# Kernel tuning notes

Measured on AMD Instinct MI355X. Metric: run time of the kernel, lower is better.

## Reference

```python
import jax, jax.numpy as jnp
import numpy as np

N_E = 8192
E_DIM = 64
BETA = 0.25
DIVERSITY_GAMMA = 1.0
INV_TEMP = 100.0
EPS = 1e-05


def _entropy(p):
    # matches torch: (-p * log(clamp(p, min=eps))).sum(-1)
    return (-p * jnp.log(jnp.clip(p, EPS))).sum(axis=-1)


def setup_inputs() -> dict:
    key = jax.random.key(0)
    k1, k2 = jax.random.split(key)
    z = jax.random.normal(k1, (16, E_DIM, 32, 32), dtype=jnp.float32)
    # codebook, init like nn.Embedding then uniform_(-1/n_e, 1/n_e) scale doesn't matter for math;
    # use a small uniform init faithful to the module
    emb = jax.random.uniform(k2, (N_E, E_DIM), dtype=jnp.float32,
                             minval=-1.0 / N_E, maxval=1.0 / N_E)
    return {"z": z, "emb": emb}


def reference(z, emb):
    sg = jax.lax.stop_gradient
    # b c h w -> b h w c
    zp = jnp.transpose(z, (0, 2, 3, 1))            # [B,H,W,C]
    zf = zp.reshape(-1, E_DIM)                      # [N, C]
    # pairwise squared distances: ||z||^2 + ||e||^2 - 2 z e^T
    d = (jnp.sum(zf * zf, axis=1, keepdims=True)
         + jnp.sum(emb * emb, axis=1)
         - 2.0 * jnp.einsum('nd,kd->nk', zf, emb))  # [N, n_e]
    min_indices = jnp.argmin(d, axis=1)             # [N]
    z_q = emb[min_indices].reshape(zp.shape)        # gather, [B,H,W,C]
    # legacy commitment loss
    loss = (jnp.mean((sg(z_q) - zp) ** 2)
            + BETA * jnp.mean((z_q - sg(zp)) ** 2))
    # entropy aux loss (frac_per_sample_entropy == 1.0)
    prob = jax.nn.softmax(-d * INV_TEMP, axis=-1)   # [N, n_e]
    per_sample_entropy = _entropy(prob).mean()
    avg_prob = prob.mean(axis=0)                    # [n_e]
    codebook_entropy = _entropy(avg_prob)
    entropy_aux = per_sample_entropy - DIVERSITY_GAMMA * codebook_entropy
    # straight-through estimator
    z_q = zp + sg(z_q - zp)
    quantized = jnp.transpose(z_q, (0, 3, 1, 2))    # b h w c -> b c h w
    return quantized, loss, entropy_aux, min_indices
```

## Files before the change

### kernel.cpp

```cpp
#include <hip/hip_runtime.h>
#include <cfloat>


typedef __attribute__((ext_vector_type(8))) short short8v;
typedef __attribute__((ext_vector_type(4))) float f32x4;

#define C100L2E 144.26950408889634f
#define C200L2E 288.53900817779268f
#define LN2 0.6931471805599453

#define BLOB_TILE 33792
#define OFF_BLOB   0
#define OFF_INVZ   2162688
#define OFF_MINIDX 2228224
#define OFF_AVG    2293760
#define OFF_PSE    2326528
#define OFF_ZPART  2326544
#define OFF_S1PART (OFF_ZPART + 262144)
#define OFF_DMPART (OFF_S1PART + 262144)
#define OFF_IMPART (OFF_DMPART + 262144)
#define OFF_LOSSP  (OFF_IMPART + 262144)

__device__ __forceinline__ unsigned short f2bf_rne(float f) {
    unsigned u = __float_as_uint(f);
    u = (u + 0x7fffu + ((u >> 16) & 1u)) >> 16;
    return (unsigned short)u;
}

__device__ __forceinline__ void gload_lds16(const void* g, void* l) {
    __builtin_amdgcn_global_load_lds(
        (const __attribute__((address_space(1))) unsigned int*)g,
        (__attribute__((address_space(3))) unsigned int*)l, 16, 0, 0);
}

__global__ __launch_bounds__(256) void k_prep(const float* __restrict__ emb,
                                              char* __restrict__ blob) {
    const int k = blockIdx.x * 256 + threadIdx.x;
    const float* row = emb + k * 64;
    float fv[64];
#pragma unroll
    for (int i = 0; i < 16; ++i) {
        float4 v = ((const float4*)row)[i];
        fv[4 * i] = v.x; fv[4 * i + 1] = v.y; fv[4 * i + 2] = v.z; fv[4 * i + 3] = v.w;
    }
    float r8[8];
#pragma unroll
    for (int j = 0; j < 8; ++j) r8[j] = __fmul_rn(fv[j], fv[j]);
#pragma unroll
    for (int i = 8; i < 64; i += 8)
#pragma unroll
        for (int j = 0; j < 8; ++j)
            r8[j] = __fadd_rn(r8[j], __fmul_rn(fv[i + j], fv[i + j]));
    float s01 = __fadd_rn(r8[0], r8[1]), s23 = __fadd_rn(r8[2], r8[3]);
    float s45 = __fadd_rn(r8[4], r8[5]), s67 = __fadd_rn(r8[6], r8[7]);
    float e2 = __fadd_rn(__fadd_rn(s01, s23), __fadd_rn(s45, s67));

    char* tb = blob + (size_t)(k >> 7) * BLOB_TILE;
    const int r = k & 127;
    ((float*)(tb + 32768))[r] = e2;
    const int sw = (r & 7) << 4;
#pragma unroll
    for (int dh = 0; dh < 2; ++dh)
#pragma unroll
        for (int cg = 0; cg < 4; ++cg) {
            short8v hv, lv;
#pragma unroll
            for (int e = 0; e < 8; ++e) {
                float f = fv[dh * 32 + cg * 8 + e];
                unsigned short hb = f2bf_rne(f);
                float hf = __uint_as_float((unsigned)hb << 16);
                hv[e] = (short)hb;
                lv[e] = (short)f2bf_rne(f - hf);
            }
            const int byt = (r * 128 + dh * 64 + cg * 16) ^ sw;
            *(short8v*)(tb + byt) = hv;
            *(short8v*)(tb + 16384 + byt) = lv;
        }
}

#define STAGE_EMB(DSTBASE, TILE)                                                  \
    {                                                                             \
        const char* gsrc = blob + (size_t)(TILE) * BLOB_TILE;                     \
        char* ldst = (DSTBASE) + ((tid >> 6) << 10);                              \
        const char* g = gsrc + tid * 16;                                          \
        _Pragma("unroll")                                                         \
        for (int q = 0; q < 8; ++q)                                               \
            gload_lds16(g + q * 4096, ldst + q * 4096);                           \
        if (tid < 32) gload_lds16(gsrc + 32768 + tid * 16, (DSTBASE) + 32768);    \
    }

__global__ __launch_bounds__(256) void k_pass1(
    const float* __restrict__ z, const char* __restrict__ blob,
    char* __restrict__ zblob,
    float* __restrict__ Zpart, float* __restrict__ S1part,
    float* __restrict__ dmpart, int* __restrict__ impart)
{
    __shared__ __align__(16) char smem[BLOB_TILE];
    __shared__ float zzsh[64];
    float (*zt)[68] = (float (*)[68])smem;

    const int tid = threadIdx.x;
    const int panel = blockIdx.x >> 2;
    const int ks = blockIdx.x & 3;
    const int n0 = panel * 64;

    {
        const int c = tid & 63, rq = (tid >> 6) * 16;
        const float* src = z + ((n0 >> 10) * 64 + c) * 1024 + (n0 & 1023) + rq;
#pragma unroll
        for (int i = 0; i < 4; ++i) {
            float4 v = ((const float4*)src)[i];
            *(float4*)&zt[c][rq + 4 * i] = v;
        }
    }
    __syncthreads();
    if (tid < 64) {
        float r8[8];
#pragma unroll
        for (int j = 0; j < 8; ++j) { float v = zt[j][tid]; r8[j] = __fmul_rn(v, v); }
#pragma unroll
        for (int i = 8; i < 64; i += 8)
#pragma unroll
            for (int j = 0; j < 8; ++j) {
                float v = zt[i + j][tid];
                r8[j] = __fadd_rn(r8[j], __fmul_rn(v, v));
            }
        float s01 = __fadd_rn(r8[0], r8[1]), s23 = __fadd_rn(r8[2], r8[3]);
        float s45 = __fadd_rn(r8[4], r8[5]), s67 = __fadd_rn(r8[6], r8[7]);
        zzsh[tid] = __fadd_rn(__fadd_rn(s01, s23), __fadd_rn(s45, s67));
    }

    const int ln = tid & 63, wv = tid >> 6;
    const int lr = ln & 15, lg = ln >> 4;

    short8v Ah[2], Al[2];
#pragma unroll
    for (int s = 0; s < 2; ++s) {
        const int row = wv * 16 + lr;
        const int db = s * 32 + lg * 8;
#pragma unroll
        for (int j = 0; j < 8; ++j) {
            float f = zt[db + j][row];
            unsigned short hb = f2bf_rne(f);
            float hf = __uint_as_float((unsigned)hb << 16);
            Ah[s][j] = (short)hb;
            Al[s][j] = (short)f2bf_rne(f - hf);
        }
    }

    if (ks == 0) {
        char* tb = zblob + (size_t)panel * 16384;
        const int rowp = wv * 16 + lr;
#pragma unroll
        for (int s = 0; s < 2; ++s) {
            const int byt = rowp * 128 + s * 64 + lg * 16;
            *(short8v*)(tb + byt) = Ah[s];
            *(short8v*)(tb + 8192 + byt) = Al[s];
        }
    }
    __syncthreads();

    float zzr[4];
#pragma unroll
    for (int rg = 0; rg < 4; ++rg) zzr[rg] = zzsh[wv * 16 + lg * 4 + rg];

    STAGE_EMB(smem, ks * 16);

    float Zp[4] = {0.f, 0.f, 0.f, 0.f}, S1p[4] = {0.f, 0.f, 0.f, 0.f};
    float dmin[4] = {FLT_MAX, FLT_MAX, FLT_MAX, FLT_MAX};
    int imin[4] = {0, 0, 0, 0};

    for (int it = 0; it < 16; ++it) {
        const int kbase = ks * 2048 + it * 128;
        __syncthreads();

        f32x4 acc[8];
#pragma unroll
        for (int f = 0; f < 8; ++f) { f32x4 zv = {0.f, 0.f, 0.f, 0.f}; acc[f] = zv; }

#pragma unroll
        for (int f = 0; f < 8; ++f) {
            const int rr = f * 16 + lr;
            const int sw2 = (rr & 7) << 4;
            short8v Bh[2], Bl[2];
#pragma unroll
            for (int s = 0; s < 2; ++s) {
                const int byt = (rr * 128 + s * 64 + lg * 16) ^ sw2;
                Bh[s] = *(const short8v*)(smem + byt);
                Bl[s] = *(const short8v*)(smem + 16384 + byt);
            }
#pragma unroll
            for (int s = 0; s < 2; ++s) {
                acc[f] = __builtin_amdgcn_mfma_f32_16x16x32_bf16(Ah[s], Bh[s], acc[f], 0, 0, 0);
                acc[f] = __builtin_amdgcn_mfma_f32_16x16x32_bf16(Ah[s], Bl[s], acc[f], 0, 0, 0);
                acc[f] = __builtin_amdgcn_mfma_f32_16x16x32_bf16(Al[s], Bh[s], acc[f], 0, 0, 0);
                acc[f] = __builtin_amdgcn_mfma_f32_16x16x32_bf16(Al[s], Bl[s], acc[f], 0, 0, 0);
            }
        }

        float e2v[8];
#pragma unroll
        for (int f = 0; f < 8; ++f)
            e2v[f] = *(const float*)(smem + 32768 + (f * 16 + lr) * 4);

        __syncthreads();
        if (it < 15) STAGE_EMB(smem, ks * 16 + it + 1);

#pragma unroll
        for (int f = 0; f < 8; ++f) {
            const float c2 = e2v[f] * C100L2E;
            const int kk = kbase + f * 16 + lr;
#pragma unroll
            for (int rg = 0; rg < 4; ++rg) {
                const float sdot = acc[f][rg];
                const float t = fmaf(sdot, C200L2E, -c2);
                const float ex = __builtin_amdgcn_exp2f(t);
                Zp[rg] += ex;
                S1p[rg] = fmaf(t, ex, S1p[rg]);
                const float dnp = __fsub_rn(__fadd_rn(zzr[rg], e2v[f]),
                                            __fmul_rn(2.f, sdot));
                if (dnp < dmin[rg]) { dmin[rg] = dnp; imin[rg] = kk; }
            }
        }
    }

#pragma unroll
    for (int msk = 1; msk < 16; msk <<= 1) {
#pragma unroll
        for (int rg = 0; rg < 4; ++rg) {
            float d2 = __shfl_xor(dmin[rg], msk, 16);
            int i2 = __shfl_xor(imin[rg], msk, 16);
            float Z2 = __shfl_xor(Zp[rg], msk, 16);
            float s2 = __shfl_xor(S1p[rg], msk, 16);
            if (d2 < dmin[rg] || (d2 == dmin[rg] && i2 < imin[rg])) {
                dmin[rg] = d2; imin[rg] = i2;
            }
            Zp[rg] += Z2;
            S1p[rg] += s2;
        }
    }
    if (lr == 0) {
#pragma unroll
        for (int rg = 0; rg < 4; ++rg) {
            const int n = n0 + wv * 16 + lg * 4 + rg;
            Zpart[ks * 16384 + n] = Zp[rg];
            S1part[ks * 16384 + n] = S1p[rg];
            dmpart[ks * 16384 + n] = dmin[rg];
            impart[ks * 16384 + n] = imin[rg];
        }
    }
}

__global__ __launch_bounds__(256) void k_rowred(
    const float* __restrict__ Zpart, const float* __restrict__ S1part,
    const float* __restrict__ dmpart, const int* __restrict__ impart,
    float* __restrict__ invZ, int* __restrict__ minidx,
    float* __restrict__ out_idx, double* __restrict__ pse_sum)
{
    const int n = blockIdx.x * 256 + threadIdx.x;
    float Z = __fadd_rn(__fadd_rn(Zpart[n], Zpart[16384 + n]),
                        __fadd_rn(Zpart[32768 + n], Zpart[49152 + n]));
    float S1 = __fadd_rn(__fadd_rn(S1part[n], S1part[16384 + n]),
                         __fadd_rn(S1part[32768 + n], S1part[49152 + n]));
    float dm = dmpart[n];
    int im = impart[n];
#pragma unroll
    for (int ksp = 1; ksp < 4; ++ksp) {
        float d2 = dmpart[ksp * 16384 + n];
        int i2 = impart[ksp * 16384 + n];
        if (d2 < dm || (d2 == dm && i2 < im)) { dm = d2; im = i2; }
    }
    minidx[n] = im;
    out_idx[n] = (float)im;
    float iz = 1.0f / Z;
    invZ[n] = iz;
    double h = log((double)Z) - LN2 * (double)S1 * (double)iz;
#pragma unroll
    for (int m = 32; m > 0; m >>= 1) h += __shfl_xor(h, m, 64);
    if ((threadIdx.x & 63) == 0) atomicAdd(pse_sum, h);
}

__global__ __launch_bounds__(256) void k_pass2(
    const char* __restrict__ zblob, const char* __restrict__ blob,
    const float* __restrict__ invZ, float* __restrict__ avg_acc)
{
    __shared__ __align__(16) char smem[BLOB_TILE + 4096];
    float* izAll = (float*)(smem + BLOB_TILE);

    const int tid = threadIdx.x;
    const int kt = blockIdx.x & 63;
    const int ns = blockIdx.x >> 6;
    const int ln = tid & 63, wv = tid >> 6;
    const int lr = ln & 15, lg = ln >> 4;

    STAGE_EMB(smem, kt);
    gload_lds16((const char*)(invZ + ns * 1024) + tid * 16,
                (char*)izAll + (wv << 10));
    __syncthreads();

    float e2v[8];
#pragma unroll
    for (int f = 0; f < 8; ++f)
        e2v[f] = *(const float*)(smem + 32768 + (f * 16 + lr) * 4);

    float acck[8] = {0.f, 0.f, 0.f, 0.f, 0.f, 0.f, 0.f, 0.f};

    for (int it = 0; it < 8; ++it) {
        short8v Ah[2][2], Al[2][2];
        const int p64 = ns * 16 + it * 2 + (wv >> 1);
        const char* tb = zblob + (size_t)p64 * 16384;
#pragma unroll
        for (int m = 0; m < 2; ++m) {
            const int rowp = (wv & 1) * 32 + m * 16 + lr;
#pragma unroll
            for (int s = 0; s < 2; ++s) {
                const int byt = rowp * 128 + s * 64 + lg * 16;
                Ah[m][s] = *(const short8v*)(tb + byt);
                Al[m][s] = *(const short8v*)(tb + 8192 + byt);
            }
        }
        const int izb = it * 128 + wv * 32 + lg * 4;
        float4 iz0 = *(const float4*)&izAll[izb];
        float4 iz1 = *(const float4*)&izAll[izb + 16];
        float izr[2][4] = {{iz0.x, iz0.y, iz0.z, iz0.w},
                           {iz1.x, iz1.y, iz1.z, iz1.w}};

        f32x4 acc[2][8];
#pragma unroll
        for (int m = 0; m < 2; ++m)
#pragma unroll
            for (int f = 0; f < 8; ++f) {
                f32x4 zv = {0.f, 0.f, 0.f, 0.f};
                acc[m][f] = zv;
            }

#pragma unroll
        for (int f = 0; f < 8; ++f) {
            const int rr = f * 16 + lr;
            const int sw2 = (rr & 7) << 4;
            short8v Bh[2], Bl[2];
#pragma unroll
            for (int s = 0; s < 2; ++s) {
                const int byt = (rr * 128 + s * 64 + lg * 16) ^ sw2;
                Bh[s] = *(const short8v*)(smem + byt);
                Bl[s] = *(const short8v*)(smem + 16384 + byt);
            }
#pragma unroll
            for (int s = 0; s < 2; ++s)
#pragma unroll
                for (int m = 0; m < 2; ++m) {
                    acc[m][f] = __builtin_amdgcn_mfma_f32_16x16x32_bf16(Ah[m][s], Bh[s], acc[m][f], 0, 0, 0);
                    acc[m][f] = __builtin_amdgcn_mfma_f32_16x16x32_bf16(Ah[m][s], Bl[s], acc[m][f], 0, 0, 0);
                    acc[m][f] = __builtin_amdgcn_mfma_f32_16x16x32_bf16(Al[m][s], Bh[s], acc[m][f], 0, 0, 0);
                    acc[m][f] = __builtin_amdgcn_mfma_f32_16x16x32_bf16(Al[m][s], Bl[s], acc[m][f], 0, 0, 0);
                }
        }

#pragma unroll
        for (int f = 0; f < 8; ++f) {
            const float c2 = e2v[f] * C100L2E;
#pragma unroll
            for (int m = 0; m < 2; ++m)
#pragma unroll
                for (int rg = 0; rg < 4; ++rg) {
                    const float t = fmaf(acc[m][f][rg], C200L2E, -c2);
                    const float ex = __builtin_amdgcn_exp2f(t);
                    acck[f] = fmaf(ex, izr[m][rg], acck[f]);
                }
        }
    }

#pragma unroll
    for (int f = 0; f < 8; ++f) {
        float cs = acck[f];
        cs += __shfl_xor(cs, 16, 64);
        cs += __shfl_xor(cs, 32, 64);
        if (lg == 0) atomicAdd(&avg_acc[kt * 128 + f * 16 + lr], cs);
    }
}

__global__ __launch_bounds__(256) void k_quant(
    const float* __restrict__ z, const float* __restrict__ emb,
    const int* __restrict__ minidx, float* __restrict__ out,
    double* __restrict__ loss_part)
{
    __shared__ float lred[4];
    const int o = blockIdx.x * 256 + threadIdx.x;
    const int n = ((o >> 16) << 10) + (o & 1023);
    const int c = (o >> 10) & 63;
    const int idx = minidx[n];
    const float e = emb[idx * 64 + c];
    const float zv = z[o];
    out[o] = e;
    float d = e - zv;
    float sq = d * d;
#pragma unroll
    for (int m = 32; m > 0; m >>= 1) sq += __shfl_xor(sq, m, 64);
    if ((threadIdx.x & 63) == 0) lred[threadIdx.x >> 6] = sq;
    __syncthreads();
    if (threadIdx.x == 0)
        loss_part[blockIdx.x] = (double)lred[0] + (double)lred[1]
                              + (double)lred[2] + (double)lred[3];
}

__global__ __launch_bounds__(256) void k_final(
    const float* __restrict__ avg_acc, const double* __restrict__ pse_sum,
    const double* __restrict__ loss_part, float* __restrict__ out)
{
    __shared__ double red[256];
    const int tid = threadIdx.x;

    double lsum = 0.0;
    for (int k = tid; k < 4096; k += 256) lsum += loss_part[k];
    red[tid] = lsum;
    __syncthreads();
    for (int s = 128; s > 0; s >>= 1) {
        if (tid < s) red[tid] += red[tid + s];
        __syncthreads();
    }
    double ltot = red[0];
    __syncthreads();

    double local = 0.0;
    for (int k = tid; k < 8192; k += 256) {
        float p = avg_acc[k] * (1.0f / 16384.0f);
        float cl = fmaxf(p, 1e-5f);
        local += (double)(-p * logf(cl));
    }
    red[tid] = local;
    __syncthreads();
    for (int s = 128; s > 0; s >>= 1) {
        if (tid < s) red[tid] += red[tid + s];
        __syncthreads();
    }
    if (tid == 0) {
        double ce = red[0];
        double pse = pse_sum[0] / 16384.0;
        out[1048576] = (float)(1.25 * ltot / 1048576.0);
        out[1048577] = (float)(pse - ce);
    }
}

extern "C" void kernel_launch(void* const* d_in, const int* in_sizes, int n_in,
                              void* d_out, int out_size, void* d_ws, size_t ws_size,
                              hipStream_t stream) {
    const float* z = (const float*)d_in[0];
    const float* emb = (const float*)d_in[1];
    float* out = (float*)d_out;
    char* ws = (char*)d_ws;
    char* blob = ws + OFF_BLOB;
    float* invZ = (float*)(ws + OFF_INVZ);
    int* minidx = (int*)(ws + OFF_MINIDX);
    float* avg_acc = (float*)(ws + OFF_AVG);
    double* pse_sum = (double*)(ws + OFF_PSE);
    float* Zpart = (float*)(ws + OFF_ZPART);
    float* S1part = (float*)(ws + OFF_S1PART);
    float* dmpart = (float*)(ws + OFF_DMPART);
    int* impart = (int*)(ws + OFF_IMPART);
    double* loss_part = (double*)(ws + OFF_LOSSP);
    char* zblob = (char*)d_out;

    hipMemsetAsync(ws + OFF_AVG, 0, 32768 + 16, stream);

    k_prep<<<32, 256, 0, stream>>>(emb, blob);
    k_pass1<<<1024, 256, 0, stream>>>(z, blob, zblob, Zpart, S1part, dmpart, impart);
    k_rowred<<<64, 256, 0, stream>>>(Zpart, S1part, dmpart, impart,
                                     invZ, minidx, out + 1048578, pse_sum);
    k_pass2<<<1024, 256, 0, stream>>>(zblob, blob, invZ, avg_acc);
    k_quant<<<4096, 256, 0, stream>>>(z, emb, minidx, out, loss_part);
    k_final<<<1, 256, 0, stream>>>(avg_acc, pse_sum, loss_part, out);
}
```

Before: 187.5 us.

## Hoist z prep into own kernel, enlarge pass1 blocks, double-buffer codebook LDS

```diff
diff --git a/kernel.cpp b/kernel.cpp
--- a/kernel.cpp
+++ b/kernel.cpp
@@ -20,6 +20,7 @@
 #define OFF_DMPART (OFF_S1PART + 262144)
 #define OFF_IMPART (OFF_DMPART + 262144)
 #define OFF_LOSSP  (OFF_IMPART + 262144)
+#define OFF_ZZ     (OFF_LOSSP + 32768)
 
 __device__ __forceinline__ unsigned short f2bf_rne(float f) {
     unsigned u = __float_as_uint(f);
@@ -76,6 +77,45 @@
             *(short8v*)(tb + byt) = hv;
             *(short8v*)(tb + 16384 + byt) = lv;
         }
+}
+
+__global__ __launch_bounds__(256) void k_zprep(const float* __restrict__ z,
+                                               char* __restrict__ zblob,
+                                               float* __restrict__ zz) {
+    const int r = blockIdx.x * 256 + threadIdx.x;
+    const float* src = z + (r >> 10) * 65536 + (r & 1023);
+    float fv[64];
+#pragma unroll
+    for (int c = 0; c < 64; ++c) fv[c] = src[c * 1024];
+
+    float r8[8];
+#pragma unroll
+    for (int j = 0; j < 8; ++j) r8[j] = __fmul_rn(fv[j], fv[j]);
+#pragma unroll
+    for (int i = 8; i < 64; i += 8)
+#pragma unroll
+        for (int j = 0; j < 8; ++j)
+            r8[j] = __fadd_rn(r8[j], __fmul_rn(fv[i + j], fv[i + j]));
+    float s01 = __fadd_rn(r8[0], r8[1]), s23 = __fadd_rn(r8[2], r8[3]);
+    float s45 = __fadd_rn(r8[4], r8[5]), s67 = __fadd_rn(r8[6], r8[7]);
+    zz[r] = __fadd_rn(__fadd_rn(s01, s23), __fadd_rn(s45, s67));
+
+    char* tb = zblob + (size_t)(r >> 6) * 16384;
+    const int rowp = r & 63;
+#pragma unroll
+    for (int cg = 0; cg < 8; ++cg) {
+        short8v hv, lv;
+#pragma unroll
+        for (int e = 0; e < 8; ++e) {
+            float f = fv[cg * 8 + e];
+            unsigned short hb = f2bf_rne(f);
+            float hf = __uint_as_float((unsigned)hb << 16);
+            hv[e] = (short)hb;
+            lv[e] = (short)f2bf_rne(f - hf);
+        }
+        *(short8v*)(tb + rowp * 128 + cg * 16) = hv;
+        *(short8v*)(tb + 8192 + rowp * 128 + cg * 16) = lv;
+    }
 }
 
 #define STAGE_EMB(DSTBASE, TILE)                                                  \
@@ -89,82 +129,51 @@
         if (tid < 32) gload_lds16(gsrc + 32768 + tid * 16, (DSTBASE) + 32768);    \
     }
 
-__global__ __launch_bounds__(256) void k_pass1(
-    const float* __restrict__ z, const char* __restrict__ blob,
-    char* __restrict__ zblob,
+#define STAGE512(DSTBASE, TILE)                                                   \
+    {                                                                             \
+        const char* gsrc = blob + (size_t)(TILE) * BLOB_TILE;                     \
+        char* ldst = (DSTBASE) + ((tid >> 6) << 12);                              \
+        const char* g = gsrc + ((tid >> 6) << 12) + (tid & 63) * 16;              \
+        _Pragma("unroll")                                                         \
+        for (int q = 0; q < 4; ++q)                                               \
+            gload_lds16(g + q * 1024, ldst + q * 1024);                           \
+        if (tid < 32) gload_lds16(gsrc + 32768 + tid * 16, (DSTBASE) + 32768);    \
+    }
+
+__global__ __launch_bounds__(512) void k_pass1(
+    const char* __restrict__ zblob, const char* __restrict__ blob,
+    const float* __restrict__ zz,
     float* __restrict__ Zpart, float* __restrict__ S1part,
     float* __restrict__ dmpart, int* __restrict__ impart)
 {
-    __shared__ __align__(16) char smem[BLOB_TILE];
-    __shared__ float zzsh[64];
-    float (*zt)[68] = (float (*)[68])smem;
+    __shared__ __align__(16) char smem[2 * BLOB_TILE];
 
     const int tid = threadIdx.x;
     const int panel = blockIdx.x >> 2;
     const int ks = blockIdx.x & 3;
-    const int n0 = panel * 64;
-
-    {
-        const int c = tid & 63, rq = (tid >> 6) * 16;
-        const float* src = z + ((n0 >> 10) * 64 + c) * 1024 + (n0 & 1023) + rq;
-#pragma unroll
-        for (int i = 0; i < 4; ++i) {
-            float4 v = ((const float4*)src)[i];
-            *(float4*)&zt[c][rq + 4 * i] = v;
-        }
-    }
-    __syncthreads();
-    if (tid < 64) {
-        float r8[8];
-#pragma unroll
-        for (int j = 0; j < 8; ++j) { float v = zt[j][tid]; r8[j] = __fmul_rn(v, v); }
-#pragma unroll
-        for (int i = 8; i < 64; i += 8)
-#pragma unroll
-            for (int j = 0; j < 8; ++j) {
-                float v = zt[i + j][tid];
-                r8[j] = __fadd_rn(r8[j], __fmul_rn(v, v));
-            }
-        float s01 = __fadd_rn(r8[0], r8[1]), s23 = __fadd_rn(r8[2], r8[3]);
-        float s45 = __fadd_rn(r8[4], r8[5]), s67 = __fadd_rn(r8[6], r8[7]);
-        zzsh[tid] = __fadd_rn(__fadd_rn(s01, s23), __fadd_rn(s45, s67));
-    }
+    const int n0 = panel * 128;
 
     const int ln = tid & 63, wv = tid >> 6;
     const int lr = ln & 15, lg = ln >> 4;
 
     short8v Ah[2], Al[2];
-#pragma unroll
-    for (int s = 0; s < 2; ++s) {
-        const int row = wv * 16 + lr;
-        const int db = s * 32 + lg * 8;
-#pragma unroll
-        for (int j = 0; j < 8; ++j) {
-            float f = zt[db + j][row];
-            unsigned short hb = f2bf_rne(f);
-            float hf = __uint_as_float((unsigned)hb << 16);
-            Ah[s][j] = (short)hb;
-            Al[s][j] = (short)f2bf_rne(f - hf);
-        }
-    }
-
-    if (ks == 0) {
-        char* tb = zblob + (size_t)panel * 16384;
-        const int rowp = wv * 16 + lr;
+    {
+        const int p64 = (n0 >> 6) + (wv >> 2);
+        const int rowp = (wv & 3) * 16 + lr;
+        const char* tb = zblob + (size_t)p64 * 16384;
 #pragma unroll
         for (int s = 0; s < 2; ++s) {
             const int byt = rowp * 128 + s * 64 + lg * 16;
-            *(short8v*)(tb + byt) = Ah[s];
-            *(short8v*)(tb + 8192 + byt) = Al[s];
-        }
-    }
-    __syncthreads();
-
+            Ah[s] = *(const short8v*)(tb + byt);
+            Al[s] = *(const short8v*)(tb + 8192 + byt);
+        }
+    }
     float zzr[4];
 #pragma unroll
-    for (int rg = 0; rg < 4; ++rg) zzr[rg] = zzsh[wv * 16 + lg * 4 + rg];
-
-    STAGE_EMB(smem, ks * 16);
+    for (int rg = 0; rg < 4; ++rg)
+        zzr[rg] = zz[n0 + wv * 16 + lg * 4 + rg];
+
+    STAGE512(smem, ks * 16);
 
     float Zp[4] = {0.f, 0.f, 0.f, 0.f}, S1p[4] = {0.f, 0.f, 0.f, 0.f};
     float dmin[4] = {FLT_MAX, FLT_MAX, FLT_MAX, FLT_MAX};
@@ -173,6 +182,8 @@
     for (int it = 0; it < 16; ++it) {
         const int kbase = ks * 2048 + it * 128;
         __syncthreads();
+        const char* bb = smem + (it & 1) * BLOB_TILE;
+        if (it < 15) STAGE512(smem + ((it + 1) & 1) * BLOB_TILE, ks * 16 + it + 1);
 
         f32x4 acc[8];
 #pragma unroll
@@ -186,8 +197,8 @@
 #pragma unroll
             for (int s = 0; s < 2; ++s) {
                 const int byt = (rr * 128 + s * 64 + lg * 16) ^ sw2;
-                Bh[s] = *(const short8v*)(smem + byt);
-                Bl[s] = *(const short8v*)(smem + 16384 + byt);
+                Bh[s] = *(const short8v*)(bb + byt);
+                Bl[s] = *(const short8v*)(bb + 16384 + byt);
             }
 #pragma unroll
             for (int s = 0; s < 2; ++s) {
@@ -198,17 +209,10 @@
             }
         }
 
-        float e2v[8];
-#pragma unroll
-        for (int f = 0; f < 8; ++f)
-            e2v[f] = *(const float*)(smem + 32768 + (f * 16 + lr) * 4);
-
-        __syncthreads();
-        if (it < 15) STAGE_EMB(smem, ks * 16 + it + 1);
-
 #pragma unroll
         for (int f = 0; f < 8; ++f) {
-            const float c2 = e2v[f] * C100L2E;
+            const float e2v = *(const float*)(bb + 32768 + (f * 16 + lr) * 4);
+            const float c2 = e2v * C100L2E;
             const int kk = kbase + f * 16 + lr;
 #pragma unroll
             for (int rg = 0; rg < 4; ++rg) {
@@ -217,8 +221,8 @@
                 const float ex = __builtin_amdgcn_exp2f(t);
                 Zp[rg] += ex;
                 S1p[rg] = fmaf(t, ex, S1p[rg]);
-                const float dnp = __fsub_rn(__fadd_rn(zzr[rg], e2v[f]),
-                                            __fmul_rn(2.f, sdot));
+                const float pre = __fadd_rn(zzr[rg], e2v);
+                const float dnp = fmaf(-2.f, sdot, pre);
                 if (dnp < dmin[rg]) { dmin[rg] = dnp; imin[rg] = kk; }
             }
         }
@@ -458,12 +462,14 @@
     float* dmpart = (float*)(ws + OFF_DMPART);
     int* impart = (int*)(ws + OFF_IMPART);
     double* loss_part = (double*)(ws + OFF_LOSSP);
+    float* zz = (float*)(ws + OFF_ZZ);
     char* zblob = (char*)d_out;
 
     hipMemsetAsync(ws + OFF_AVG, 0, 32768 + 16, stream);
 
     k_prep<<<32, 256, 0, stream>>>(emb, blob);
-    k_pass1<<<1024, 256, 0, stream>>>(z, blob, zblob, Zpart, S1part, dmpart, impart);
+    k_zprep<<<64, 256, 0, stream>>>(z, zblob, zz);
+    k_pass1<<<512, 512, 0, stream>>>(zblob, blob, zz, Zpart, S1part, dmpart, impart);
     k_rowred<<<64, 256, 0, stream>>>(Zpart, S1part, dmpart, impart,
                                      invZ, minidx, out + 1048578, pse_sum);
     k_pass2<<<1024, 256, 0, stream>>>(zblob, blob, invZ, avg_acc);
```

After: 187.3 us. Within noise of the previous version (-0.1%).
